# Kernel tuning notes

Measured on AMD Instinct MI355X. Metric: run time of the kernel, lower is better.

Reference implementation:

```python
import jax, jax.numpy as jnp
import numpy as np

B, S, D, H = 2, 2048, 1024, 16
HD = D // H  # 64


def setup_inputs() -> dict:
    key = jax.random.key(0)
    ks = jax.random.split(key, 11)
    sc = 1.0 / np.sqrt(D)
    return {
        "query": jax.random.normal(ks[0], (B, S, D), jnp.float32),
        "key_in": jax.random.normal(ks[1], (B, S, D), jnp.float32),
        "value_in": jax.random.normal(ks[2], (B, S, D), jnp.float32),
        "mask": jnp.ones((1, 1, S, S), dtype=bool),
        "Wq": jax.random.normal(ks[3], (D, D), jnp.float32) * sc,
        "bq": jnp.zeros((D,), jnp.float32),
        "Wk": jax.random.normal(ks[4], (D, D), jnp.float32) * sc,
        "bk": jnp.zeros((D,), jnp.float32),
        "Wv": jax.random.normal(ks[5], (D, D), jnp.float32) * sc,
        "bv": jnp.zeros((D,), jnp.float32),
        "Wo": jax.random.normal(ks[6], (D, D), jnp.float32) * sc,
        "bo": jnp.zeros((D,), jnp.float32),
    }


def _split_heads(x):
    b, s, _ = x.shape
    return x.reshape(b, s, H, HD).transpose(0, 2, 1, 3)  # [B,H,S,HD]


def reference(query, key_in, value_in, mask, Wq, bq, Wk, bk, Wv, bv, Wo, bo):
    # linear projections (torch Linear: x @ W.T + b)
    q = _split_heads(query @ Wq.T + bq)
    k = _split_heads(key_in @ Wk.T + bk)
    v = _split_heads(value_in @ Wv.T + bv)
    scores = jnp.einsum("bhqd,bhkd->bhqk", q, k) / np.sqrt(HD).astype(np.float32)
    scores = jnp.where(mask == 0, jnp.float32(-1e20), scores)
    probs = jax.nn.softmax(scores, axis=-1)
    attn = jnp.einsum("bhqk,bhkd->bhqd", probs, v)  # [B,H,S,HD]
    combined = attn.transpose(0, 2, 1, 3).reshape(query.shape[0], query.shape[1], H * HD)
    return combined @ Wo.T + bo
```

## Files before the change

### kernel.cpp

```cpp
#include <hip/hip_runtime.h>

#define B_  2
#define S_  2048
#define D_  1024
#define H_  16
#define HD_ 64

typedef float          f32x4 __attribute__((ext_vector_type(4)));
typedef short          s16x8 __attribute__((ext_vector_type(8)));
typedef unsigned short u16x4 __attribute__((ext_vector_type(4)));
typedef unsigned int   u32x2 __attribute__((ext_vector_type(2)));
typedef unsigned int   u32x4 __attribute__((ext_vector_type(4)));

static __device__ __forceinline__ unsigned short f2bf(float f) {
  unsigned int u = __builtin_bit_cast(unsigned int, f);
  u += 0x7FFFu + ((u >> 16) & 1u);
  return (unsigned short)(u >> 16);
}

static __device__ __forceinline__ unsigned cvt_pk_bf16(float lo, float hi) {
  unsigned r;
  asm("v_cvt_pk_bf16_f32 %0, %1, %2" : "=v"(r) : "v"(lo), "v"(hi));
  return r;
}

#define GLDS16(g, l)                                                        \
  __builtin_amdgcn_global_load_lds(                                         \
      (const __attribute__((address_space(1))) void*)(g),                   \
      (__attribute__((address_space(3))) void*)(l), 16, 0, 0)

struct ConvSet {
  const float* s[4];
  unsigned short* d[4];
  int n[4];
};

__global__ __launch_bounds__(256) void conv_kernel(ConvSet cs) {
  const int idx = blockIdx.y;
  const int i = (blockIdx.x * 256 + threadIdx.x) * 8;
  if (i >= cs.n[idx]) return;
  const float* s = cs.s[idx];
  unsigned short* d = cs.d[idx];
  f32x4 a = *(const f32x4*)(s + i);
  f32x4 b = *(const f32x4*)(s + i + 4);
  u32x4 o;
  o[0] = cvt_pk_bf16(a[0], a[1]);
  o[1] = cvt_pk_bf16(a[2], a[3]);
  o[2] = cvt_pk_bf16(b[0], b[1]);
  o[3] = cvt_pk_bf16(b[2], b[3]);
  *(u32x4*)(d + i) = o;
}

template <int XM, bool PERM>
__global__ __launch_bounds__(256) void gemm_bf16(
    const void* __restrict__ X0, const void* __restrict__ X1,
    const void* __restrict__ X2,
    const unsigned short* __restrict__ W0, const unsigned short* __restrict__ W1,
    const unsigned short* __restrict__ W2,
    const float* __restrict__ b0, const float* __restrict__ b1, const float* __restrict__ b2,
    void* __restrict__ o0, void* __restrict__ o1, void* __restrict__ o2)
{
  constexpr int K = D_, N = D_;
  constexpr int NKS = K / 32;
  const int z = blockIdx.z;
  const void* X           = z == 0 ? X0 : (z == 1 ? X1 : X2);
  const unsigned short* W = z == 0 ? W0 : (z == 1 ? W1 : W2);
  const float* bias       = z == 0 ? b0 : (z == 1 ? b1 : b2);
  void* outp              = z == 0 ? o0 : (z == 1 ? o1 : o2);

  __shared__ unsigned short As[2][128][32];
  __shared__ unsigned short Bs[2][128][32];

  const int t = threadIdx.x, lane = t & 63, w = t >> 6;
  const int wr = w >> 1, wc = w & 1;
  const int Lb = blockIdx.y * 8 + blockIdx.x;
  const int m0 = (Lb & 31) * 128;
  const int n0 = (Lb >> 5) * 128;
  const int lg = lane >> 4, lr = lane & 15;

  const int srow = w * 32 + (lane >> 2);
  const int scol = (lane & 3) * 8;
  const unsigned short* Bsrc = W + (size_t)(n0 + srow) * K + scol;
  const unsigned short* Asrc =
      (XM == 0) ? (const unsigned short*)X + (size_t)(m0 + srow) * K + scol : nullptr;
  const int arow0 = t >> 3;
  const int acol  = (t & 7) * 4;
  const float* Xf = (XM == 1) ? (const float*)X : nullptr;

  f32x4 acc[4][4];
#pragma unroll
  for (int i = 0; i < 4; ++i)
#pragma unroll
    for (int j = 0; j < 4; ++j) acc[i][j] = f32x4{0.f, 0.f, 0.f, 0.f};

  if (XM == 0) {
#pragma unroll
    for (int i = 0; i < 2; ++i)
      GLDS16(Asrc + (size_t)i * 16 * K, &As[0][w * 32 + i * 16][0]);
  } else {
#pragma unroll
    for (int i = 0; i < 4; ++i) {
      f32x4 v = *(const f32x4*)(Xf + (size_t)(m0 + arow0 + 32 * i) * K + acol);
      u32x2 p;
      p[0] = cvt_pk_bf16(v[0], v[1]);
      p[1] = cvt_pk_bf16(v[2], v[3]);
      *(u32x2*)&As[0][arow0 + 32 * i][acol] = p;
    }
  }
#pragma unroll
  for (int i = 0; i < 2; ++i)
    GLDS16(Bsrc + (size_t)i * 16 * K, &Bs[0][w * 32 + i * 16][0]);
  __syncthreads();

  for (int ks = 0; ks < NKS; ++ks) {
    const int cur = ks & 1, nxt = cur ^ 1;
    const int k1 = (ks + 1) * 32;

    f32x4 av0, av1, av2, av3;
    if (ks + 1 < NKS) {
      if (XM == 0) {
#pragma unroll
        for (int i = 0; i < 2; ++i)
          GLDS16(Asrc + k1 + (size_t)i * 16 * K, &As[nxt][w * 32 + i * 16][0]);
      } else {
        av0 = *(const f32x4*)(Xf + (size_t)(m0 + arow0)      * K + k1 + acol);
        av1 = *(const f32x4*)(Xf + (size_t)(m0 + arow0 + 32) * K + k1 + acol);
        av2 = *(const f32x4*)(Xf + (size_t)(m0 + arow0 + 64) * K + k1 + acol);
        av3 = *(const f32x4*)(Xf + (size_t)(m0 + arow0 + 96) * K + k1 + acol);
      }
#pragma unroll
      for (int i = 0; i < 2; ++i)
        GLDS16(Bsrc + k1 + (size_t)i * 16 * K, &Bs[nxt][w * 32 + i * 16][0]);
    }

    s16x8 af[4], bfr[4];
#pragma unroll
    for (int i = 0; i < 4; ++i) af[i]  = *(const s16x8*)&As[cur][wr * 64 + i * 16 + lr][lg * 8];
#pragma unroll
    for (int j = 0; j < 4; ++j) bfr[j] = *(const s16x8*)&Bs[cur][wc * 64 + j * 16 + lr][lg * 8];
#pragma unroll
    for (int i = 0; i < 4; ++i)
#pragma unroll
      for (int j = 0; j < 4; ++j)
        acc[i][j] = __builtin_amdgcn_mfma_f32_16x16x32_bf16(af[i], bfr[j], acc[i][j], 0, 0, 0);

    if (XM == 1 && ks + 1 < NKS) {
      u32x2 p0, p1, p2, p3;
      p0[0] = cvt_pk_bf16(av0[0], av0[1]); p0[1] = cvt_pk_bf16(av0[2], av0[3]);
      p1[0] = cvt_pk_bf16(av1[0], av1[1]); p1[1] = cvt_pk_bf16(av1[2], av1[3]);
      p2[0] = cvt_pk_bf16(av2[0], av2[1]); p2[1] = cvt_pk_bf16(av2[2], av2[3]);
      p3[0] = cvt_pk_bf16(av3[0], av3[1]); p3[1] = cvt_pk_bf16(av3[2], av3[3]);
      *(u32x2*)&As[nxt][arow0][acol]      = p0;
      *(u32x2*)&As[nxt][arow0 + 32][acol] = p1;
      *(u32x2*)&As[nxt][arow0 + 64][acol] = p2;
      *(u32x2*)&As[nxt][arow0 + 96][acol] = p3;
    }

    __syncthreads();
  }

#pragma unroll
  for (int i = 0; i < 4; ++i) {
    int rowb = m0 + wr * 64 + i * 16 + lg * 4;
#pragma unroll
    for (int j = 0; j < 4; ++j) {
      int col = n0 + wc * 64 + j * 16 + lr;
      float bv = bias[col];
      if (PERM) {
        unsigned short* o = (unsigned short*)outp;
        int h = col >> 6, hd = col & (HD_ - 1);
        if (z == 2) {
          int b = rowb >> 11, sv = rowb & (S_ - 1);
          u32x2 pv;
          pv[0] = cvt_pk_bf16(acc[i][j][0] + bv, acc[i][j][1] + bv);
          pv[1] = cvt_pk_bf16(acc[i][j][2] + bv, acc[i][j][3] + bv);
          *(u32x2*)(o + ((size_t)((b * H_ + h) * HD_ + hd)) * S_ + sv) = pv;
        } else {
#pragma unroll
          for (int r = 0; r < 4; ++r) {
            int rr = rowb + r;
            int b = rr >> 11, s = rr & (S_ - 1);
            o[(((size_t)(b * H_ + h)) * S_ + s) * HD_ + hd] = f2bf(acc[i][j][r] + bv);
          }
        }
      } else {
#pragma unroll
        for (int r = 0; r < 4; ++r)
          ((float*)outp)[(size_t)(rowb + r) * N + col] = acc[i][j][r] + bv;
      }
    }
  }
}

template <bool XF32, bool PERM>
__global__ __launch_bounds__(256) void gemm_kernel(
    const void* __restrict__ X0, const void* __restrict__ X1, const void* __restrict__ X2,
    const float* __restrict__ W0, const float* __restrict__ W1, const float* __restrict__ W2,
    const float* __restrict__ b0, const float* __restrict__ b1, const float* __restrict__ b2,
    void* __restrict__ o0, void* __restrict__ o1, void* __restrict__ o2)
{
  constexpr int K = D_, N = D_;
  const int z = blockIdx.z;
  const void*  Xv   = z == 0 ? X0 : (z == 1 ? X1 : X2);
  const float* W    = z == 0 ? W0 : (z == 1 ? W1 : W2);
  const float* bias = z == 0 ? b0 : (z == 1 ? b1 : b2);
  void*        outp = z == 0 ? o0 : (z == 1 ? o1 : o2);

  __shared__ unsigned short As[128][32];
  __shared__ unsigned short Bs[128][32];

  const int t = threadIdx.x, lane = t & 63, w = t >> 6;
  const int wr = w >> 1, wc = w & 1;
  const int Lb = blockIdx.y * 8 + blockIdx.x;
  const int m0 = (Lb & 31) * 128;
  const int n0 = (Lb >> 5) * 128;
  const int lg = lane >> 4, lr = lane & 15;

  f32x4 acc[4][4];
#pragma unroll
  for (int i = 0; i < 4; ++i)
#pragma unroll
    for (int j = 0; j < 4; ++j) acc[i][j] = f32x4{0.f, 0.f, 0.f, 0.f};

  for (int k0 = 0; k0 < K; k0 += 32) {
    __syncthreads();
#pragma unroll
    for (int i = 0; i < 4; ++i) {
      int c = t + 256 * i;
      int row = c >> 3, ko = (c & 7) * 4;
      if (XF32) {
        const float* Xf = (const float*)Xv;
        f32x4 v = *(const f32x4*)(Xf + (size_t)(m0 + row) * K + k0 + ko);
        u16x4 p;
#pragma unroll
        for (int j = 0; j < 4; ++j) p[j] = f2bf(v[j]);
        *(u16x4*)&As[row][ko] = p;
      } else {
        const unsigned short* Xu = (const unsigned short*)Xv;
        *(u16x4*)&As[row][ko] = *(const u16x4*)(Xu + (size_t)(m0 + row) * K + k0 + ko);
      }
    }
#pragma unroll
    for (int i = 0; i < 4; ++i) {
      int c = t + 256 * i;
      int row = c >> 3, ko = (c & 7) * 4;
      f32x4 v = *(const f32x4*)(W + (size_t)(n0 + row) * K + k0 + ko);
      u16x4 p;
#pragma unroll
      for (int j = 0; j < 4; ++j) p[j] = f2bf(v[j]);
      *(u16x4*)&Bs[row][ko] = p;
    }
    __syncthreads();

    s16x8 af[4], bfr[4];
#pragma unroll
    for (int i = 0; i < 4; ++i) af[i]  = *(const s16x8*)&As[wr * 64 + i * 16 + lr][lg * 8];
#pragma unroll
    for (int j = 0; j < 4; ++j) bfr[j] = *(const s16x8*)&Bs[wc * 64 + j * 16 + lr][lg * 8];
#pragma unroll
    for (int i = 0; i < 4; ++i)
#pragma unroll
      for (int j = 0; j < 4; ++j)
        acc[i][j] = __builtin_amdgcn_mfma_f32_16x16x32_bf16(af[i], bfr[j], acc[i][j], 0, 0, 0);
  }

#pragma unroll
  for (int i = 0; i < 4; ++i) {
    int rowb = m0 + wr * 64 + i * 16 + lg * 4;
#pragma unroll
    for (int j = 0; j < 4; ++j) {
      int col = n0 + wc * 64 + j * 16 + lr;
      float bv = bias[col];
      if (PERM) {
        unsigned short* o = (unsigned short*)outp;
        int h = col >> 6, hd = col & (HD_ - 1);
        if (z == 2) {
          int b = rowb >> 11, sv = rowb & (S_ - 1);
          u16x4 pv;
#pragma unroll
          for (int r = 0; r < 4; ++r) pv[r] = f2bf(acc[i][j][r] + bv);
          *(u16x4*)(o + ((size_t)((b * H_ + h) * HD_ + hd)) * S_ + sv) = pv;
        } else {
#pragma unroll
          for (int r = 0; r < 4; ++r) {
            int rr = rowb + r;
            int b = rr >> 11, s = rr & (S_ - 1);
            o[(((size_t)(b * H_ + h)) * S_ + s) * HD_ + hd] = f2bf(acc[i][j][r] + bv);
          }
        }
      } else {
#pragma unroll
        for (int r = 0; r < 4; ++r)
          ((float*)outp)[(size_t)(rowb + r) * N + col] = acc[i][j][r] + bv;
      }
    }
  }
}

__global__ __launch_bounds__(256) void attn_kernel(
    const unsigned short* __restrict__ Q,
    const unsigned short* __restrict__ Kg,
    const unsigned short* __restrict__ VT,
    unsigned short* __restrict__ O)
{
  __shared__ unsigned short Ks[2][64][64];
  __shared__ unsigned short Vt[2][64][64];
  __shared__ unsigned int   Pw32[4][16][32];

  const int t = threadIdx.x, lane = t & 63, w = t >> 6;
  const int lg = lane >> 4, lr = lane & 15;
  const int Lb = blockIdx.y * 32 + blockIdx.x;
  const int bh = Lb & 31;
  const int qblk = Lb >> 5;
  const int q0 = qblk * 64 + w * 16;
  const size_t baseK = (size_t)bh * S_ * HD_;
  const size_t baseV = (size_t)bh * HD_ * S_;

  s16x8 qa[2];
#pragma unroll
  for (int kc = 0; kc < 2; ++kc)
    qa[kc] = *(const s16x8*)(Q + baseK + (size_t)(q0 + lr) * HD_ + kc * 32 + lg * 8);

  const int sub = lane >> 3;
  const int cg  = (lane & 7) ^ sub;
  const unsigned short* Ksrc = Kg + baseK + (size_t)(w * 16 + sub) * HD_ + cg * 8;
  const unsigned short* Vsrc = VT + baseV + (size_t)(w * 16 + sub) * S_  + cg * 8;

  f32x4 po[4];
#pragma unroll
  for (int nb = 0; nb < 4; ++nb) po[nb] = f32x4{0.f, 0.f, 0.f, 0.f};
  float m_r = -1e30f, l_r = 0.f;
  const float C2 = 0.18033688f;
  const int   xs = (lr & 7) * 8;
  const int   xw = (lr & 7) * 4;

  constexpr int NT = S_ / 64;

  {
    GLDS16(Ksrc,                    &Ks[0][w * 16][0]);
    GLDS16(Ksrc + 8 * HD_,          &Ks[0][w * 16 + 8][0]);
    GLDS16(Vsrc,                    &Vt[0][w * 16][0]);
    GLDS16(Vsrc + (size_t)8 * S_,   &Vt[0][w * 16 + 8][0]);
  }
  __syncthreads();

#pragma unroll 2
  for (int kt = 0; kt < NT; ++kt) {
    const int cur = kt & 1;
    if (kt + 1 < NT) {
      const int nxt = cur ^ 1;
      const size_t ko = (size_t)(kt + 1) * 64 * HD_;
      const size_t vo = (size_t)(kt + 1) * 64;
      GLDS16(Ksrc + ko,                  &Ks[nxt][w * 16][0]);
      GLDS16(Ksrc + ko + 8 * HD_,        &Ks[nxt][w * 16 + 8][0]);
      GLDS16(Vsrc + vo,                  &Vt[nxt][w * 16][0]);
      GLDS16(Vsrc + vo + (size_t)8 * S_, &Vt[nxt][w * 16 + 8][0]);
    }

    f32x4 sf[4];
    __builtin_amdgcn_s_setprio(1);
#pragma unroll
    for (int nb = 0; nb < 4; ++nb) {
      f32x4 a = f32x4{0.f, 0.f, 0.f, 0.f};
      int row = nb * 16 + lr;
#pragma unroll
      for (int kc = 0; kc < 2; ++kc) {
        s16x8 kb = *(const s16x8*)&Ks[cur][row][(kc * 32 + lg * 8) ^ xs];
        a = __builtin_amdgcn_mfma_f32_16x16x32_bf16(kb, qa[kc], a, 0, 0, 0);
      }
      sf[nb] = a;
    }
    __builtin_amdgcn_s_setprio(0);

    float mx = sf[0][0];
#pragma unroll
    for (int nb = 0; nb < 4; ++nb)
#pragma unroll
      for (int r = 0; r < 4; ++r) mx = fmaxf(mx, sf[nb][r]);
    mx = fmaxf(mx, __shfl_xor(mx, 16));
    mx = fmaxf(mx, __shfl_xor(mx, 32));
    float ms = mx * C2;
    bool grow = (ms - m_r) > 8.f;
    if (__any(grow)) {
      float mn = fmaxf(m_r, ms);
      float alpha = __builtin_amdgcn_exp2f(m_r - mn);
      m_r = mn;
      l_r *= alpha;
#pragma unroll
      for (int nb = 0; nb < 4; ++nb)
#pragma unroll
        for (int r = 0; r < 4; ++r) po[nb][r] *= alpha;
    }

    float pr[4][4];
    float rs = 0.f;
#pragma unroll
    for (int nb = 0; nb < 4; ++nb)
#pragma unroll
      for (int r = 0; r < 4; ++r) {
        float p = __builtin_amdgcn_exp2f(fmaf(sf[nb][r], C2, -m_r));
        pr[nb][r] = p;
        rs += p;
      }
    rs += __shfl_xor(rs, 16);
    rs += __shfl_xor(rs, 32);
    l_r += rs;

#pragma unroll
    for (int nb = 0; nb < 4; ++nb)
#pragma unroll
      for (int half = 0; half < 2; ++half) {
        unsigned pk = cvt_pk_bf16(pr[nb][2 * half], pr[nb][2 * half + 1]);
        Pw32[w][lr][(nb * 8 + lg * 2 + half) ^ xw] = pk;
      }
    asm volatile("s_waitcnt lgkmcnt(0)" ::: "memory");
    __builtin_amdgcn_sched_barrier(0);
    s16x8 pa[2];
#pragma unroll
    for (int kc = 0; kc < 2; ++kc)
      pa[kc] = *(const s16x8*)&Pw32[w][lr][(kc * 16 + lg * 4) ^ xw];

    __builtin_amdgcn_s_setprio(1);
#pragma unroll
    for (int nb = 0; nb < 4; ++nb) {
      int d = nb * 16 + lr;
#pragma unroll
      for (int kc = 0; kc < 2; ++kc) {
        s16x8 vb = *(const s16x8*)&Vt[cur][d][(kc * 32 + lg * 8) ^ xs];
        po[nb] = __builtin_amdgcn_mfma_f32_16x16x32_bf16(vb, pa[kc], po[nb], 0, 0, 0);
      }
    }
    __builtin_amdgcn_s_setprio(0);

    __syncthreads();
  }

  unsigned* Ot = (unsigned*)&Ks[0][0][0];
  {
    float inv = __builtin_amdgcn_rcpf(l_r);
    const int qlocal = w * 16 + lr;
#pragma unroll
    for (int nb = 0; nb < 4; ++nb)
#pragma unroll
      for (int half = 0; half < 2; ++half) {
        unsigned pk = cvt_pk_bf16(po[nb][2 * half] * inv, po[nb][2 * half + 1] * inv);
        Ot[qlocal * 32 + ((nb * 8 + lg * 2 + half) ^ xw)] = pk;
      }
  }
  __syncthreads();
  {
    const int qp = t >> 2, ch = t & 3;
    const int xq = (qp & 7) * 4;
    u32x4 r0 = *(const u32x4*)&Ot[qp * 32 + ((ch * 8) ^ xq)];
    u32x4 r1 = *(const u32x4*)&Ot[qp * 32 + ((ch * 8 + 4) ^ xq)];
    const int b = bh >> 4, h = bh & (H_ - 1);
    size_t s = (size_t)qblk * 64 + qp;
    unsigned short* o = O + ((size_t)b * S_ + s) * D_ + h * HD_ + ch * 16;
    *(u32x4*)o = r0;
    *(u32x4*)(o + 8) = r1;
  }
}

extern "C" void kernel_launch(void* const* d_in, const int* in_sizes, int n_in,
                              void* d_out, int out_size, void* d_ws, size_t ws_size,
                              hipStream_t stream) {
  const float* query    = (const float*)d_in[0];
  const float* key_in   = (const float*)d_in[1];
  const float* value_in = (const float*)d_in[2];
  const float* Wq = (const float*)d_in[4];
  const float* bq = (const float*)d_in[5];
  const float* Wk = (const float*)d_in[6];
  const float* bk = (const float*)d_in[7];
  const float* Wv = (const float*)d_in[8];
  const float* bv = (const float*)d_in[9];
  const float* Wo = (const float*)d_in[10];
  const float* bo = (const float*)d_in[11];

  const size_t NA = (size_t)B_ * S_ * D_;
  const size_t NW = (size_t)D_ * D_;
  dim3 blk(256);

  if (ws_size >= (4 * NA + 4 * NW) * sizeof(unsigned short)) {
    unsigned short* Wb[4];
    Wb[0] = (unsigned short*)d_ws;
    Wb[1] = Wb[0] + NW;
    Wb[2] = Wb[1] + NW;
    Wb[3] = Wb[2] + NW;
    unsigned short* Qp = Wb[3] + NW;
    unsigned short* Kp = Qp + NA;
    unsigned short* Vp = Kp + NA;
    unsigned short* Ao = Vp + NA;

    ConvSet cs;
    cs.s[0] = Wq; cs.d[0] = Wb[0]; cs.n[0] = (int)NW;
    cs.s[1] = Wk; cs.d[1] = Wb[1]; cs.n[1] = (int)NW;
    cs.s[2] = Wv; cs.d[2] = Wb[2]; cs.n[2] = (int)NW;
    cs.s[3] = Wo; cs.d[3] = Wb[3]; cs.n[3] = (int)NW;
    conv_kernel<<<dim3((unsigned)(NW / (256 * 8)), 4), blk, 0, stream>>>(cs);

    gemm_bf16<1, true><<<dim3(8, 32, 3), blk, 0, stream>>>(
        query, key_in, value_in, Wb[0], Wb[1], Wb[2], bq, bk, bv, Qp, Kp, Vp);
    attn_kernel<<<dim3(S_ / 64, B_ * H_), blk, 0, stream>>>(Qp, Kp, Vp, Ao);
    gemm_bf16<0, false><<<dim3(8, 32, 1), blk, 0, stream>>>(
        Ao, nullptr, nullptr, Wb[3], nullptr, nullptr, bo, nullptr, nullptr,
        (float*)d_out, nullptr, nullptr);
  } else {
    unsigned short* Qp = (unsigned short*)d_ws;
    unsigned short* Kp = Qp + NA;
    unsigned short* Vp = Kp + NA;
    unsigned short* Ao = Vp + NA;
    gemm_kernel<true, true><<<dim3(8, 32, 3), blk, 0, stream>>>(
        query, key_in, value_in, Wq, Wk, Wv, bq, bk, bv, Qp, Kp, Vp);
    attn_kernel<<<dim3(S_ / 64, B_ * H_), blk, 0, stream>>>(Qp, Kp, Vp, Ao);
    gemm_kernel<false, false><<<dim3(8, 32, 1), blk, 0, stream>>>(
        Ao, nullptr, nullptr, Wo, nullptr, nullptr, bo, nullptr, nullptr,
        (float*)d_out, nullptr, nullptr);
  }
}
```

Measured before the change: 259.7 us.

## Pre-convert activations to bf16 in conv kernel and fuse softmax P stores

When the workspace is large enough, a new path converts the query, key and value activations to bf16 in the same batched conversion launch as the weights. The QKV projection GEMM then runs with template mode 0 on bf16 inputs instead of converting fp32 on the fly, and the attention output reuses the query buffer. Separately, the attention softmax now computes the max with a tree reduction and packs and stores P to LDS right after each exp, which removes the intermediate array. The cost is an extra read and write pass over the activations and a larger workspace requirement.

```diff
diff --git a/kernel.cpp b/kernel.cpp
--- a/kernel.cpp
+++ b/kernel.cpp
@@ -30,9 +30,9 @@
       (__attribute__((address_space(3))) void*)(l), 16, 0, 0)
 
 struct ConvSet {
-  const float* s[4];
-  unsigned short* d[4];
-  int n[4];
+  const float* s[7];
+  unsigned short* d[7];
+  int n[7];
 };
 
 __global__ __launch_bounds__(256) void conv_kernel(ConvSet cs) {
@@ -372,11 +372,11 @@
     }
     __builtin_amdgcn_s_setprio(0);
 
-    float mx = sf[0][0];
-#pragma unroll
-    for (int nb = 0; nb < 4; ++nb)
-#pragma unroll
-      for (int r = 0; r < 4; ++r) mx = fmaxf(mx, sf[nb][r]);
+    float mxa = fmaxf(fmaxf(sf[0][0], sf[0][1]), fmaxf(sf[0][2], sf[0][3]));
+    float mxb = fmaxf(fmaxf(sf[1][0], sf[1][1]), fmaxf(sf[1][2], sf[1][3]));
+    float mxc = fmaxf(fmaxf(sf[2][0], sf[2][1]), fmaxf(sf[2][2], sf[2][3]));
+    float mxd = fmaxf(fmaxf(sf[3][0], sf[3][1]), fmaxf(sf[3][2], sf[3][3]));
+    float mx = fmaxf(fmaxf(mxa, mxb), fmaxf(mxc, mxd));
     mx = fmaxf(mx, __shfl_xor(mx, 16));
     mx = fmaxf(mx, __shfl_xor(mx, 32));
     float ms = mx * C2;
@@ -392,27 +392,22 @@
         for (int r = 0; r < 4; ++r) po[nb][r] *= alpha;
     }
 
-    float pr[4][4];
-    float rs = 0.f;
-#pragma unroll
-    for (int nb = 0; nb < 4; ++nb)
-#pragma unroll
-      for (int r = 0; r < 4; ++r) {
-        float p = __builtin_amdgcn_exp2f(fmaf(sf[nb][r], C2, -m_r));
-        pr[nb][r] = p;
-        rs += p;
-      }
+    float rsn[4];
+#pragma unroll
+    for (int nb = 0; nb < 4; ++nb) {
+      float p0 = __builtin_amdgcn_exp2f(fmaf(sf[nb][0], C2, -m_r));
+      float p1 = __builtin_amdgcn_exp2f(fmaf(sf[nb][1], C2, -m_r));
+      float p2 = __builtin_amdgcn_exp2f(fmaf(sf[nb][2], C2, -m_r));
+      float p3 = __builtin_amdgcn_exp2f(fmaf(sf[nb][3], C2, -m_r));
+      Pw32[w][lr][(nb * 8 + lg * 2)     ^ xw] = cvt_pk_bf16(p0, p1);
+      Pw32[w][lr][(nb * 8 + lg * 2 + 1) ^ xw] = cvt_pk_bf16(p2, p3);
+      rsn[nb] = (p0 + p1) + (p2 + p3);
+    }
+    float rs = (rsn[0] + rsn[1]) + (rsn[2] + rsn[3]);
     rs += __shfl_xor(rs, 16);
     rs += __shfl_xor(rs, 32);
     l_r += rs;
 
-#pragma unroll
-    for (int nb = 0; nb < 4; ++nb)
-#pragma unroll
-      for (int half = 0; half < 2; ++half) {
-        unsigned pk = cvt_pk_bf16(pr[nb][2 * half], pr[nb][2 * half + 1]);
-        Pw32[w][lr][(nb * 8 + lg * 2 + half) ^ xw] = pk;
-      }
     asm volatile("s_waitcnt lgkmcnt(0)" ::: "memory");
     __builtin_amdgcn_sched_barrier(0);
     s16x8 pa[2];
@@ -480,7 +475,38 @@
   const size_t NW = (size_t)D_ * D_;
   dim3 blk(256);
 
-  if (ws_size >= (4 * NA + 4 * NW) * sizeof(unsigned short)) {
+  if (ws_size >= (6 * NA + 4 * NW) * sizeof(unsigned short)) {
+    unsigned short* Wb[4];
+    Wb[0] = (unsigned short*)d_ws;
+    Wb[1] = Wb[0] + NW;
+    Wb[2] = Wb[1] + NW;
+    Wb[3] = Wb[2] + NW;
+    unsigned short* Xb[3];
+    Xb[0] = Wb[3] + NW;
+    Xb[1] = Xb[0] + NA;
+    Xb[2] = Xb[1] + NA;
+    unsigned short* Qp = Xb[2] + NA;
+    unsigned short* Kp = Qp + NA;
+    unsigned short* Vp = Kp + NA;
+    unsigned short* Ao = Xb[0];
+
+    ConvSet cs;
+    cs.s[0] = Wq; cs.d[0] = Wb[0]; cs.n[0] = (int)NW;
+    cs.s[1] = Wk; cs.d[1] = Wb[1]; cs.n[1] = (int)NW;
+    cs.s[2] = Wv; cs.d[2] = Wb[2]; cs.n[2] = (int)NW;
+    cs.s[3] = Wo; cs.d[3] = Wb[3]; cs.n[3] = (int)NW;
+    cs.s[4] = query;    cs.d[4] = Xb[0]; cs.n[4] = (int)NA;
+    cs.s[5] = key_in;   cs.d[5] = Xb[1]; cs.n[5] = (int)NA;
+    cs.s[6] = value_in; cs.d[6] = Xb[2]; cs.n[6] = (int)NA;
+    conv_kernel<<<dim3((unsigned)(NA / (256 * 8)), 7), blk, 0, stream>>>(cs);
+
+    gemm_bf16<0, true><<<dim3(8, 32, 3), blk, 0, stream>>>(
+        Xb[0], Xb[1], Xb[2], Wb[0], Wb[1], Wb[2], bq, bk, bv, Qp, Kp, Vp);
+    attn_kernel<<<dim3(S_ / 64, B_ * H_), blk, 0, stream>>>(Qp, Kp, Vp, Ao);
+    gemm_bf16<0, false><<<dim3(8, 32, 1), blk, 0, stream>>>(
+        Ao, nullptr, nullptr, Wb[3], nullptr, nullptr, bo, nullptr, nullptr,
+        (float*)d_out, nullptr, nullptr);
+  } else if (ws_size >= (4 * NA + 4 * NW) * sizeof(unsigned short)) {
     unsigned short* Wb[4];
     Wb[0] = (unsigned short*)d_ws;
     Wb[1] = Wb[0] + NW;
```

Measured after the change: 257.5 us. No clear change (-0.9%).
